# Kernel optimization log

Hardware: AMD Instinct MI355X
Metric: run time of the kernel (lower is better)

Reference implementation:

```python
import jax, jax.numpy as jnp
import numpy as np

N = 100_000      # nodes
E = 1_600_000    # edges (avg degree 16)
D_IN = 128
D_OUT = 128
K = 64           # low-rank attention rank


def setup_inputs() -> dict:
    key = jax.random.key(0)
    ks = jax.random.split(key, 6)
    s = lambda d: 1.0 / np.sqrt(d)
    return {
        "x": jax.random.normal(ks[0], (N, D_IN), dtype=jnp.float32),
        "edge_index": jax.random.randint(ks[1], (2, E), 0, N, dtype=jnp.int32),
        "W_gcn": jax.random.normal(ks[2], (D_IN, D_OUT), dtype=jnp.float32) * s(D_IN),
        "b_gcn": jnp.zeros((D_OUT,), jnp.float32),
        "W_att": jax.random.normal(ks[3], (D_IN, 4 * K), dtype=jnp.float32) * s(D_IN),
        "b_att": jnp.zeros((4 * K,), jnp.float32),
        "W_red": jax.random.normal(ks[4], (D_OUT + 2 * K, D_OUT), dtype=jnp.float32) * s(D_OUT + 2 * K),
        "b_red": jnp.zeros((D_OUT,), jnp.float32),
    }


def _forward(x, W_gcn, b_gcn, W_att, b_att, W_red, b_red, edge_index):
    n = x.shape[0]
    # --- GCN conv (symmetric normalization, self-loops), dropout = identity (eval) ---
    loop = jnp.arange(n, dtype=edge_index.dtype)
    src = jnp.concatenate([edge_index[0], loop])
    dst = jnp.concatenate([edge_index[1], loop])
    deg = jax.ops.segment_sum(jnp.ones_like(dst, dtype=x.dtype), dst, num_segments=n)
    dinv = jax.lax.rsqrt(deg)                      # deg >= 1 due to self-loops
    norm = dinv[src] * dinv[dst]                   # [E+n]
    h = x @ W_gcn                                  # [n, D_OUT]
    agg = jax.ops.segment_sum(h[src] * norm[:, None], dst, num_segments=n) + b_gcn
    x_local = jax.nn.relu(agg)

    # --- Low-rank global attention (LRGA) ---
    t = jax.nn.relu(x @ W_att + b_att)             # [n, 4K]
    U, V, Z, T = jnp.split(t, 4, axis=1)           # each [n, K]
    # joint_normalize2: scalar 1/mean(U @ (V^T @ 1_n))
    D = 1.0 / jnp.mean(U @ (V.T @ jnp.ones((n, 1), x.dtype)))
    res = (U @ (V.T @ Z)) * D                      # [n, K]
    x_global = jnp.concatenate([res, T], axis=1)   # [n, 2K]

    # --- fuse + dim reduce ---
    return jnp.concatenate([x_local, x_global], axis=1) @ W_red + b_red


def reference(x, edge_index, W_gcn, b_gcn, W_att, b_att, W_red, b_red):
    return _forward(x, W_gcn, b_gcn, W_att, b_att, W_red, b_red, edge_index)
```

## Files before the change

kernel.cpp:

```cpp
#include <hip/hip_runtime.h>

#define DIN   128
#define DOUT  128
#define KR    64
#define TCOLS 256
#define WCOLS 384
#define P_RED 1024
#define PSTR  4224
#define STCAP 6144

typedef unsigned short ushort_t;
typedef __attribute__((ext_vector_type(8))) short bf16x8;
typedef __attribute__((ext_vector_type(4))) float f32x4;

__device__ __forceinline__ float bf2f(unsigned short u) {
  return __uint_as_float(((unsigned int)u) << 16);
}
__device__ __forceinline__ unsigned short f2bf(float f) {
  unsigned int b = __float_as_uint(f);
  b = b + 0x7FFFu + ((b >> 16) & 1u);
  return (unsigned short)(b >> 16);
}

__global__ __launch_bounds__(256) void k_init(int* __restrict__ degc, float* __restrict__ VtZ,
                                              float* __restrict__ colsum, int* __restrict__ bcur,
                                              int* __restrict__ ocnt, int N) {
  int i = blockIdx.x * 256 + threadIdx.x;
  if (i < N) degc[i] = 1;
  if (i < 4096) VtZ[i] = 0.f;
  if (i < 128) colsum[i] = 0.f;
  if (i < 128) bcur[i] = 0;
  if (i == 0) ocnt[0] = 0;
}

__global__ __launch_bounds__(256) void k_deg(const int* __restrict__ ei, int* __restrict__ degc, int E) {
  int e = blockIdx.x * 256 + threadIdx.x;
  if (e < E) atomicAdd(&degc[ei[E + e]], 1);
}

__global__ __launch_bounds__(256) void k_split(const float* __restrict__ x,
                                               ushort_t* __restrict__ xhF, ushort_t* __restrict__ xloF,
                                               int N, int total_slots) {
  int gid = blockIdx.x * 256 + threadIdx.x;
  int stride = gridDim.x * 256;
  for (; gid < total_slots; gid += stride) {
    int f = gid >> 6, l = gid & 63;
    int r16 = f >> 2, s = f & 3;
    int row = r16 * 16 + (l & 15);
    int k = s * 32 + ((l >> 4) << 3);
    ushort4 h0, h1, l0, l1;
    if (row < N) {
      float4 a = *(const float4*)&x[(size_t)row * DIN + k];
      float4 b = *(const float4*)&x[(size_t)row * DIN + k + 4];
      h0.x = f2bf(a.x); h0.y = f2bf(a.y); h0.z = f2bf(a.z); h0.w = f2bf(a.w);
      h1.x = f2bf(b.x); h1.y = f2bf(b.y); h1.z = f2bf(b.z); h1.w = f2bf(b.w);
      l0.x = f2bf(a.x - bf2f(h0.x)); l0.y = f2bf(a.y - bf2f(h0.y));
      l0.z = f2bf(a.z - bf2f(h0.z)); l0.w = f2bf(a.w - bf2f(h0.w));
      l1.x = f2bf(b.x - bf2f(h1.x)); l1.y = f2bf(b.y - bf2f(h1.y));
      l1.z = f2bf(b.z - bf2f(h1.z)); l1.w = f2bf(b.w - bf2f(h1.w));
    } else {
      h0 = make_ushort4(0, 0, 0, 0); h1 = h0; l0 = h0; l1 = h0;
    }
    ((ushort4*)xhF)[gid * 2] = h0;
    ((ushort4*)xhF)[gid * 2 + 1] = h1;
    ((ushort4*)xloF)[gid * 2] = l0;
    ((ushort4*)xloF)[gid * 2 + 1] = l1;
  }
}

__global__ __launch_bounds__(256) void k_wprep(const float* __restrict__ Wg, const float* __restrict__ Wa,
                                               ushort_t* __restrict__ whF, ushort_t* __restrict__ wlF) {
  int g = blockIdx.x * 256 + threadIdx.x;
  int f = g >> 6, l = g & 63;
  int c16 = f >> 2, s = f & 3;
  int col = c16 * 16 + (l & 15);
  int k = s * 32 + ((l >> 4) << 3);
#pragma unroll
  for (int j = 0; j < 8; ++j) {
    float v = (col < DOUT) ? Wg[(size_t)(k + j) * DOUT + col]
                           : Wa[(size_t)(k + j) * TCOLS + (col - DOUT)];
    ushort_t h = f2bf(v);
    whF[(size_t)g * 8 + j] = h;
    wlF[(size_t)g * 8 + j] = f2bf(v - bf2f(h));
  }
}

__global__ __launch_bounds__(256) void k_scan1(const int* __restrict__ degc, int* __restrict__ offs,
                                               int* __restrict__ bsums, int N) {
  __shared__ int s[256];
  int tid = threadIdx.x;
  int base = blockIdx.x * 1024 + tid * 4;
  int c[4], e[4];
#pragma unroll
  for (int q = 0; q < 4; ++q) c[q] = (base + q < N) ? (degc[base + q] - 1) : 0;
  e[0] = 0; e[1] = c[0]; e[2] = e[1] + c[1]; e[3] = e[2] + c[2];
  int tsum = e[3] + c[3];
  s[tid] = tsum; __syncthreads();
  for (int off = 1; off < 256; off <<= 1) {
    int v = (tid >= off) ? s[tid - off] : 0;
    __syncthreads();
    s[tid] += v;
    __syncthreads();
  }
  int tb = s[tid] - tsum;
#pragma unroll
  for (int q = 0; q < 4; ++q) if (base + q < N) offs[base + q] = tb + e[q];
  if (tid == 255) bsums[blockIdx.x] = s[255];
}

__global__ __launch_bounds__(128) void k_scan2(const int* __restrict__ bsums, int* __restrict__ boff,
                                               int* __restrict__ offs, int NBLK, int N) {
  __shared__ int s[128];
  int tid = threadIdx.x;
  int v = (tid < NBLK) ? bsums[tid] : 0;
  s[tid] = v; __syncthreads();
  for (int off = 1; off < 128; off <<= 1) {
    int u = (tid >= off) ? s[tid - off] : 0;
    __syncthreads();
    s[tid] += u;
    __syncthreads();
  }
  boff[tid] = s[tid] - v;
  if (tid == 127) offs[N] = s[127];
}

__global__ __launch_bounds__(256) void k_scan3(int* __restrict__ offs, const int* __restrict__ boff,
                                               const int* __restrict__ degc, float* __restrict__ dinv,
                                               int* __restrict__ cursor, int N) {
  int i = blockIdx.x * 256 + threadIdx.x;
  if (i < N) {
    offs[i] += boff[i >> 10];
    dinv[i] = rsqrtf((float)degc[i]);
    cursor[i] = 0;
  }
}

__global__ __launch_bounds__(256) void k_bin(const int* __restrict__ ei, int* __restrict__ bcur,
                                             int2* __restrict__ buckets,
                                             int2* __restrict__ oflow, int* __restrict__ ocnt,
                                             int E, int B, int CAP) {
  __shared__ int hist[128], pref[128], place[128], gbase[128];
  __shared__ int2 st[4096];
  int tid = threadIdx.x;
  int e0 = blockIdx.x * 4096;
  int nE = min(4096, E - e0);
  if (nE <= 0) return;

  if (tid < 128) { hist[tid] = 0; place[tid] = 0; }
  __syncthreads();

  int src[16], dst[16];
#pragma unroll
  for (int q = 0; q < 16; ++q) {
    int idx = tid + q * 256;
    if (idx < nE) {
      src[q] = ei[e0 + idx];
      dst[q] = ei[E + e0 + idx];
      atomicAdd(&hist[dst[q] >> 10], 1);
    }
  }
  __syncthreads();

  if (tid < 128) pref[tid] = hist[tid];
  __syncthreads();
  for (int off = 1; off < 128; off <<= 1) {
    int v = (tid < 128 && tid >= off) ? pref[tid - off] : 0;
    __syncthreads();
    if (tid < 128) pref[tid] += v;
    __syncthreads();
  }
  if (tid < 128) pref[tid] -= hist[tid];
  if (tid < B && hist[tid] > 0) gbase[tid] = atomicAdd(&bcur[tid], hist[tid]);
  __syncthreads();

#pragma unroll
  for (int q = 0; q < 16; ++q) {
    int idx = tid + q * 256;
    if (idx < nE) {
      int b = dst[q] >> 10;
      int p = pref[b] + atomicAdd(&place[b], 1);
      st[p] = make_int2(src[q], dst[q]);
    }
  }
  __syncthreads();

  for (int i = tid; i < nE; i += 256) {
    int2 q = st[i];
    int b = q.y >> 10;
    int gp = gbase[b] + (i - pref[b]);
    if (gp < CAP) {
      buckets[(size_t)b * CAP + gp] = q;
    } else {
      int oi = atomicAdd(ocnt, 1);
      oflow[oi] = q;
    }
  }
}

__global__ __launch_bounds__(256) void k_scatter2(const int2* __restrict__ buckets,
                                                  const int* __restrict__ bcur,
                                                  const int* __restrict__ offs,
                                                  const float* __restrict__ dinv,
                                                  int* __restrict__ cursor,
                                                  int2* __restrict__ csr, int CAP, int N) {
  __shared__ int lcur[256];
  __shared__ int2 st[STCAP];
  int cb = blockIdx.x >> 2;
  int lo = cb * 1024 + (blockIdx.x & 3) * 256;
  if (lo >= N) return;
  int tid = threadIdx.x;
  int nnode = min(256, N - lo);
  int base = offs[lo];
  int nb = offs[lo + nnode] - base;
  if (tid < nnode) lcur[tid] = offs[lo + tid];
  __syncthreads();
  int avail = min(bcur[cb], CAP);
  const int2* sp = &buckets[(size_t)cb * CAP];
  bool staged = (nb <= STCAP);
  int quarter = lo >> 8;
  for (int i = tid; i < avail; i += 256) {
    int2 q = sp[i];
    if ((q.y >> 8) != quarter) continue;
    int p = atomicAdd(&lcur[q.y - lo], 1);
    int2 c;
    c.x = q.x;
    c.y = __float_as_int(dinv[q.x] * dinv[q.y]);
    if (staged) st[p - base] = c;
    else        csr[p] = c;
  }
  __syncthreads();
  if (staged) {
    for (int i = tid; i < nb; i += 256) csr[base + i] = st[i];
  }
  if (tid < nnode) cursor[lo + tid] = lcur[tid];
}

__global__ __launch_bounds__(256) void k_fixup(const int2* __restrict__ oflow, const int* __restrict__ ocnt,
                                               int* __restrict__ cursor, const float* __restrict__ dinv,
                                               int2* __restrict__ csr) {
  int n = ocnt[0];
  for (int i = blockIdx.x * 256 + threadIdx.x; i < n; i += gridDim.x * 256) {
    int2 q = oflow[i];
    int pos = atomicAdd(&cursor[q.y], 1);
    int2 c;
    c.x = q.x;
    c.y = __float_as_int(dinv[q.x] * dinv[q.y]);
    csr[pos] = c;
  }
}

#define LOADK(S, AH, AL, BH, BL)                                              \
  {                                                                           \
    _Pragma("unroll") for (int m_ = 0; m_ < 4; ++m_) {                        \
      size_t fo_ = (((size_t)(r16b + m_) * 4 + (S)) * 64 + lane) * 8;         \
      AH[m_] = *(const bf16x8*)&xhF[fo_];                                     \
      AL[m_] = *(const bf16x8*)&xloF[fo_];                                    \
    }                                                                         \
    _Pragma("unroll") for (int n_ = 0; n_ < 4; ++n_) {                        \
      size_t fo_ = (((size_t)(c16b + n_) * 4 + (S)) * 64 + lane) * 8;         \
      BH[n_] = *(const bf16x8*)&whF[fo_];                                     \
      BL[n_] = *(const bf16x8*)&wlF[fo_];                                     \
    }                                                                         \
  }

__global__ __launch_bounds__(256) void k_gemm1_mfma(const ushort_t* __restrict__ xhF,
                                                    const ushort_t* __restrict__ xloF,
                                                    const ushort_t* __restrict__ whF,
                                                    const ushort_t* __restrict__ wlF,
                                                    const float* __restrict__ ba,
                                                    ushort_t* __restrict__ hs, ushort_t* __restrict__ t,
                                                    int N, int ntiles) {
  int bid = blockIdx.x;
  int g = bid / 24;
  int rem = bid - g * 24;
  int colblk = rem >> 3;
  int ytile = g * 8 + (rem & 7);
  if (ytile >= ntiles) return;

  int tid = threadIdx.x;
  int lane = tid & 63;
  int wave = tid >> 6;
  int wr = wave >> 1, wc = wave & 1;
  int rowbase = ytile * 128 + wr * 64;
  int gcb = colblk * 128 + wc * 64;
  int r16b = ytile * 8 + wr * 4;
  int c16b = colblk * 8 + wc * 4;
  int lr = lane & 15;
  int rq = (lane >> 4) * 4;

  f32x4 acc[4][4] = {};
  bf16x8 ah[2][4], al[2][4], bh[2][4], bl[2][4];

  LOADK(0, ah[0], al[0], bh[0], bl[0]);
#pragma unroll
  for (int s = 0; s < 4; ++s) {
    int cur = s & 1, nxt = cur ^ 1;
    if (s < 3) LOADK(s + 1, ah[nxt], al[nxt], bh[nxt], bl[nxt]);
#pragma unroll
    for (int m = 0; m < 4; ++m)
#pragma unroll
      for (int n = 0; n < 4; ++n) {
        acc[m][n] = __builtin_amdgcn_mfma_f32_16x16x32_bf16(ah[cur][m], bl[cur][n], acc[m][n], 0, 0, 0);
        acc[m][n] = __builtin_amdgcn_mfma_f32_16x16x32_bf16(al[cur][m], bh[cur][n], acc[m][n], 0, 0, 0);
        acc[m][n] = __builtin_amdgcn_mfma_f32_16x16x32_bf16(ah[cur][m], bh[cur][n], acc[m][n], 0, 0, 0);
      }
  }

  if (colblk == 0) {
#pragma unroll
    for (int m = 0; m < 4; ++m)
#pragma unroll
      for (int i = 0; i < 4; ++i) {
        int row = rowbase + m * 16 + rq + i;
        if (row < N) {
#pragma unroll
          for (int n = 0; n < 4; ++n)
            hs[(size_t)row * DOUT + gcb + n * 16 + lr] = f2bf(acc[m][n][i]);
        }
      }
  } else {
    float bav[4];
#pragma unroll
    for (int n = 0; n < 4; ++n) bav[n] = ba[gcb - DOUT + n * 16 + lr];
#pragma unroll
    for (int m = 0; m < 4; ++m)
#pragma unroll
      for (int i = 0; i < 4; ++i) {
        int row = rowbase + m * 16 + rq + i;
        if (row < N) {
#pragma unroll
          for (int n = 0; n < 4; ++n)
            t[(size_t)row * TCOLS + gcb - DOUT + n * 16 + lr] =
                f2bf(fmaxf(acc[m][n][i] + bav[n], 0.f));
        }
      }
  }
}

__global__ __launch_bounds__(256) void k_red(const ushort_t* __restrict__ t, float* __restrict__ part,
                                             int N) {
  __shared__ ushort_t ts[32 * 200];
  __shared__ float csh[512];
  int tid = threadIdx.x;
  int lane = tid & 63;
  int w = tid >> 6;
  int lr = lane & 15;
  int lk = (lane >> 4) * 8;
  int vcol = 64 + w * 16 + lr;
  int col2 = lane * 2;

  f32x4 acc[4] = {};
  float cs0 = 0.f, cs1 = 0.f;
  int ntiles = (N + 31) >> 5;

  for (int tile = blockIdx.x; tile < ntiles; tile += gridDim.x) {
    int r0 = tile * 32;
    for (int i = tid; i < 768; i += 256) {
      int r = i / 24, c0 = (i % 24) * 8;
      int row = r0 + r;
      ushort4 v0, v1;
      if (row < N) {
        v0 = ((const ushort4*)&t[(size_t)row * TCOLS + c0])[0];
        v1 = ((const ushort4*)&t[(size_t)row * TCOLS + c0])[1];
      } else {
        v0 = make_ushort4(0, 0, 0, 0); v1 = v0;
      }
      *(ushort4*)&ts[r * 200 + c0] = v0;
      *(ushort4*)&ts[r * 200 + c0 + 4] = v1;
    }
    __syncthreads();
    bf16x8 a, b[4];
#pragma unroll
    for (int j = 0; j < 8; ++j)
      ((ushort_t*)&a)[j] = ts[(lk + j) * 200 + vcol];
#pragma unroll
    for (int n = 0; n < 4; ++n)
#pragma unroll
      for (int j = 0; j < 8; ++j)
        ((ushort_t*)&b[n])[j] = ts[(lk + j) * 200 + 128 + n * 16 + lr];
#pragma unroll
    for (int j = 0; j < 8; ++j) {
      ushort2 u = *(const ushort2*)&ts[(w * 8 + j) * 200 + col2];
      cs0 += bf2f(u.x); cs1 += bf2f(u.y);
    }
#pragma unroll
    for (int n = 0; n < 4; ++n)
      acc[n] = __builtin_amdgcn_mfma_f32_16x16x32_bf16(a, b[n], acc[n], 0, 0, 0);
    __syncthreads();
  }

  float* pb = &part[(size_t)blockIdx.x * PSTR];
  int rq = (lane >> 4) * 4;
#pragma unroll
  for (int n = 0; n < 4; ++n)
#pragma unroll
    for (int i = 0; i < 4; ++i)
      pb[(w * 16 + rq + i) * 64 + n * 16 + lr] = acc[n][i];

  csh[tid] = cs0;
  csh[256 + tid] = cs1;
  __syncthreads();
  if (w == 0) {
    float t0 = csh[lane] + csh[64 + lane] + csh[128 + lane] + csh[192 + lane];
    float t1 = csh[256 + lane] + csh[320 + lane] + csh[384 + lane] + csh[448 + lane];
    pb[4096 + col2] = t0;
    pb[4096 + col2 + 1] = t1;
  }
}

__global__ __launch_bounds__(256) void k_redsum(const float* __restrict__ part,
                                                float* __restrict__ VtZ, float* __restrict__ colsum) {
  __shared__ float s[256];
  int tid = threadIdx.x;
  int j = blockIdx.x * 64 + (tid & 63);
  int bc = tid >> 6;
  float a = 0.f;
#pragma unroll 4
  for (int b = bc; b < P_RED; b += 4) a += part[(size_t)b * PSTR + j];
  s[tid] = a;
  __syncthreads();
  if (bc == 0) {
    float v = s[tid] + s[tid + 64] + s[tid + 128] + s[tid + 192];
    if (j < 4096) VtZ[j] = v;
    else colsum[j - 4096] = v;
  }
}

__global__ __launch_bounds__(64) void k_d(const float* __restrict__ colsum, float* __restrict__ Dws, int N) {
  __shared__ float s[64];
  int k = threadIdx.x;
  s[k] = colsum[k] * colsum[64 + k];
  __syncthreads();
  for (int off = 32; off > 0; off >>= 1) {
    if (k < off) s[k] += s[k + off];
    __syncthreads();
  }
  if (k == 0) {
    float p = s[0];
    Dws[0] = (p != 0.f) ? ((float)N / p) : 0.f;
  }
}

__global__ __launch_bounds__(256) void k_prep(const float* __restrict__ VtZ,
                                              const float* __restrict__ Dws,
                                              const float* __restrict__ Wr,
                                              ushort_t* __restrict__ weffF) {
  int g = blockIdx.x * 256 + threadIdx.x;
  int f = g >> 6, l = g & 63;
  int c16 = f >> 3, s = f & 7;
  int c = c16 * 16 + (l & 15);
  int k0 = s * 32 + ((l >> 4) << 3);
  float Dv = Dws[0];
#pragma unroll
  for (int j = 0; j < 8; ++j) {
    int k = k0 + j;
    float v;
    if (k < 128 || k >= 192) {
      v = Wr[(size_t)k * DOUT + c];
    } else {
      int kk = k - 128;
      float acc = 0.f;
      for (int q = 0; q < 64; ++q)
        acc += VtZ[kk * 64 + q] * Wr[(size_t)(128 + q) * DOUT + c];
      v = acc * Dv;
    }
    weffF[(size_t)g * 8 + j] = f2bf(v);
  }
}

__global__ __launch_bounds__(256) void k_out_mfma(const ushort_t* __restrict__ xl,
                                                  const ushort_t* __restrict__ t,
                                                  const ushort_t* __restrict__ weffF,
                                                  const float* __restrict__ br,
                                                  float* __restrict__ out, int N) {
  __shared__ ushort_t ys[32 * 264];
  int tid = threadIdx.x;
  int lane = tid & 63;
  int w = tid >> 6;
  int lr = lane & 15;
  int lk = (lane >> 4) * 8;
  int rq = (lane >> 4) * 4;
  int r0 = blockIdx.x * 32;

  for (int i = tid; i < 1024; i += 256) {
    int r = i >> 5, c0 = (i & 31) * 8;
    int row = r0 + r;
    ushort4 v0, v1;
    if (row < N) {
      const ushort_t* src;
      if (c0 < 128)      src = &xl[(size_t)row * DOUT + c0];
      else if (c0 < 192) src = &t[(size_t)row * TCOLS + (c0 - 128)];
      else               src = &t[(size_t)row * TCOLS + c0];
      v0 = ((const ushort4*)src)[0];
      v1 = ((const ushort4*)src)[1];
    } else {
      v0 = make_ushort4(0, 0, 0, 0); v1 = v0;
    }
    *(ushort4*)&ys[r * 264 + c0] = v0;
    *(ushort4*)&ys[r * 264 + c0 + 4] = v1;
  }
  __syncthreads();

  f32x4 acc[2][2] = {};
#pragma unroll
  for (int s = 0; s < 8; ++s) {
    bf16x8 a[2], b[2];
#pragma unroll
    for (int m = 0; m < 2; ++m)
      a[m] = *(const bf16x8*)&ys[(m * 16 + lr) * 264 + s * 32 + lk];
#pragma unroll
    for (int n = 0; n < 2; ++n) {
      int f = (w * 2 + n) * 8 + s;
      b[n] = *(const bf16x8*)&weffF[((size_t)f * 64 + lane) * 8];
    }
#pragma unroll
    for (int m = 0; m < 2; ++m)
#pragma unroll
      for (int n = 0; n < 2; ++n)
        acc[m][n] = __builtin_amdgcn_mfma_f32_16x16x32_bf16(a[m], b[n], acc[m][n], 0, 0, 0);
  }

  float brv[2];
#pragma unroll
  for (int n = 0; n < 2; ++n) brv[n] = br[w * 32 + n * 16 + lr];
#pragma unroll
  for (int m = 0; m < 2; ++m)
#pragma unroll
    for (int i = 0; i < 4; ++i) {
      int row = r0 + m * 16 + rq + i;
      if (row < N) {
#pragma unroll
        for (int n = 0; n < 2; ++n)
          out[(size_t)row * DOUT + w * 32 + n * 16 + lr] = acc[m][n][i] + brv[n];
      }
    }
}

__global__ __launch_bounds__(256) void k_aggn(const ushort_t* __restrict__ hs, const int2* __restrict__ csr,
                                              const int* __restrict__ offs, const float* __restrict__ dinv,
                                              const float* __restrict__ bg,
                                              ushort_t* __restrict__ xl, int N) {
  int node = blockIdx.x * 4 + (threadIdx.x >> 6);
  int lane = threadIdx.x & 63;
  if (node >= N) return;
  int c2 = 2 * lane;
  float dn = dinv[node];
  ushort2 u = *(const ushort2*)&hs[(size_t)node * DOUT + c2];
  float a0 = dn * dn * bf2f(u.x);
  float a1 = dn * dn * bf2f(u.y);
  int e = offs[node], e1 = offs[node + 1];
  for (; e + 4 <= e1; e += 4) {
    int2 q0 = csr[e], q1 = csr[e + 1], q2 = csr[e + 2], q3 = csr[e + 3];
    ushort2 r0 = *(const ushort2*)&hs[(size_t)q0.x * DOUT + c2];
    ushort2 r1 = *(const ushort2*)&hs[(size_t)q1.x * DOUT + c2];
    ushort2 r2 = *(const ushort2*)&hs[(size_t)q2.x * DOUT + c2];
    ushort2 r3 = *(const ushort2*)&hs[(size_t)q3.x * DOUT + c2];
    float n0 = __int_as_float(q0.y), n1 = __int_as_float(q1.y);
    float n2 = __int_as_float(q2.y), n3 = __int_as_float(q3.y);
    a0 += n0 * bf2f(r0.x) + n1 * bf2f(r1.x) + n2 * bf2f(r2.x) + n3 * bf2f(r3.x);
    a1 += n0 * bf2f(r0.y) + n1 * bf2f(r1.y) + n2 * bf2f(r2.y) + n3 * bf2f(r3.y);
  }
  for (; e < e1; ++e) {
    int2 q = csr[e];
    ushort2 r = *(const ushort2*)&hs[(size_t)q.x * DOUT + c2];
    float n0 = __int_as_float(q.y);
    a0 += n0 * bf2f(r.x);
    a1 += n0 * bf2f(r.y);
  }
  ushort2 o;
  o.x = f2bf(fmaxf(a0 + bg[c2], 0.f));
  o.y = f2bf(fmaxf(a1 + bg[c2 + 1], 0.f));
  *(ushort2*)&xl[(size_t)node * DOUT + c2] = o;
}

extern "C" void kernel_launch(void* const* d_in, const int* in_sizes, int n_in,
                              void* d_out, int out_size, void* d_ws, size_t ws_size,
                              hipStream_t stream) {
  const float* x  = (const float*)d_in[0];
  const int* ei   = (const int*)d_in[1];
  const float* Wg = (const float*)d_in[2];
  const float* bg = (const float*)d_in[3];
  const float* Wa = (const float*)d_in[4];
  const float* ba = (const float*)d_in[5];
  const float* Wr = (const float*)d_in[6];
  const float* br = (const float*)d_in[7];
  float* out = (float*)d_out;

  const int N = in_sizes[0] / DIN;
  const int E = in_sizes[1] / 2;

  const int NT128 = (N + 127) / 128;
  const int N16P = NT128 * 8;
  const int NFRAG_A = N16P * 4;
  const int B = (N + 1023) >> 10;
  const int CAP = ((E / (B > 0 ? B : 1)) * 3 / 2 + 255) & ~255;

  char* p = (char*)d_ws;
  auto alloc = [&](size_t bytes) {
    char* r = p;
    p += (bytes + 255) & ~(size_t)255;
    return r;
  };
  float* Dws    = (float*)alloc(256);
  float* colsum = (float*)alloc(128 * 4);
  float* VtZ    = (float*)alloc(4096 * 4);
  int*   bsums  = (int*)alloc(1024);
  int*   boff   = (int*)alloc(1024);
  int*   bcur   = (int*)alloc(1024);
  int*   ocnt   = (int*)alloc(256);
  ushort_t* weffF = (ushort_t*)alloc(128 * 256 * 2);
  ushort_t* whF = (ushort_t*)alloc((size_t)24 * 4 * 512 * 2);
  ushort_t* wlF = (ushort_t*)alloc((size_t)24 * 4 * 512 * 2);
  float* part   = (float*)alloc((size_t)P_RED * PSTR * 4);
  int*   degc   = (int*)alloc((size_t)N * 4);
  float* dinv   = (float*)alloc((size_t)N * 4);
  int*   offs   = (int*)alloc((size_t)(N + 1) * 4);
  int*   cursor = (int*)alloc((size_t)N * 4);
  int2*  csr    = (int2*)alloc((size_t)E * 8);
  int2*  buckets= (int2*)alloc((size_t)B * CAP * 8);
  int2*  oflow  = (int2*)alloc((size_t)E * 8);
  ushort_t* xhF = (ushort_t*)alloc((size_t)NFRAG_A * 512 * 2);
  ushort_t* xloF= (ushort_t*)alloc((size_t)NFRAG_A * 512 * 2);
  ushort_t* hs  = (ushort_t*)alloc((size_t)N * DOUT * 2);
  ushort_t* t   = (ushort_t*)alloc((size_t)N * TCOLS * 2);
  ushort_t* xl  = (ushort_t*)alloc((size_t)N * DOUT * 2);
  (void)ws_size; (void)n_in; (void)out_size;

  const int GN = (N + 255) / 256;
  const int GE = (E + 255) / 256;
  const int NBLK = (N + 1023) / 1024;
  const int G1 = ((NT128 + 7) / 8) * 24;
  const int GBIN = (E + 4095) / 4096;
  const int NT32 = (N + 31) / 32;

  k_init<<<GN, 256, 0, stream>>>(degc, VtZ, colsum, bcur, ocnt, N);
  k_deg<<<GE, 256, 0, stream>>>(ei, degc, E);
  k_split<<<2048, 256, 0, stream>>>(x, xhF, xloF, N, NFRAG_A * 64);
  k_wprep<<<24, 256, 0, stream>>>(Wg, Wa, whF, wlF);
  k_scan1<<<NBLK, 256, 0, stream>>>(degc, offs, bsums, N);
  k_scan2<<<1, 128, 0, stream>>>(bsums, boff, offs, NBLK, N);
  k_scan3<<<GN, 256, 0, stream>>>(offs, boff, degc, dinv, cursor, N);
  k_bin<<<GBIN, 256, 0, stream>>>(ei, bcur, buckets, oflow, ocnt, E, B, CAP);
  k_scatter2<<<B * 4, 256, 0, stream>>>(buckets, bcur, offs, dinv, cursor, csr, CAP, N);
  k_fixup<<<32, 256, 0, stream>>>(oflow, ocnt, cursor, dinv, csr);
  k_gemm1_mfma<<<G1, 256, 0, stream>>>(xhF, xloF, whF, wlF, ba, hs, t, N, NT128);
  k_red<<<P_RED, 256, 0, stream>>>(t, part, N);
  k_redsum<<<PSTR / 64, 256, 0, stream>>>(part, VtZ, colsum);
  k_d<<<1, 64, 0, stream>>>(colsum, Dws, N);
  k_prep<<<16, 256, 0, stream>>>(VtZ, Dws, Wr, weffF);
  k_aggn<<<(N + 3) / 4, 256, 0, stream>>>(hs, csr, offs, dinv, bg, xl, N);
  k_out_mfma<<<NT32, 256, 0, stream>>>(xl, t, weffF, br, out, N);
}
```

Before: 446.0 us.

## Fuse degree count into binning and aggregation into output GEMM

The degree atomics move into k_bin, which now runs before the scan, so the separate k_deg pass over the edge list goes away. The GCN neighbor aggregation is fused into the output MFMA kernel: each block aggregates its 32 rows directly into shared memory instead of writing and re-reading the bf16 x_local buffer. This removes two launches and one intermediate round trip through global memory. In exchange the gather now runs at 32 rows per block with 8 serial rows per wave, which lowers parallelism for the latency-bound gather.

```diff
diff --git a/kernel.cpp b/kernel.cpp
--- a/kernel.cpp
+++ b/kernel.cpp
@@ -31,11 +31,6 @@
   if (i < 128) colsum[i] = 0.f;
   if (i < 128) bcur[i] = 0;
   if (i == 0) ocnt[0] = 0;
-}
-
-__global__ __launch_bounds__(256) void k_deg(const int* __restrict__ ei, int* __restrict__ degc, int E) {
-  int e = blockIdx.x * 256 + threadIdx.x;
-  if (e < E) atomicAdd(&degc[ei[E + e]], 1);
 }
 
 __global__ __launch_bounds__(256) void k_split(const float* __restrict__ x,
@@ -136,6 +131,7 @@
 }
 
 __global__ __launch_bounds__(256) void k_bin(const int* __restrict__ ei, int* __restrict__ bcur,
+                                             int* __restrict__ degc,
                                              int2* __restrict__ buckets,
                                              int2* __restrict__ oflow, int* __restrict__ ocnt,
                                              int E, int B, int CAP) {
@@ -157,6 +153,7 @@
       src[q] = ei[e0 + idx];
       dst[q] = ei[E + e0 + idx];
       atomicAdd(&hist[dst[q] >> 10], 1);
+      atomicAdd(&degc[dst[q]], 1);
     }
   }
   __syncthreads();
@@ -468,11 +465,15 @@
   }
 }
 
-__global__ __launch_bounds__(256) void k_out_mfma(const ushort_t* __restrict__ xl,
-                                                  const ushort_t* __restrict__ t,
-                                                  const ushort_t* __restrict__ weffF,
-                                                  const float* __restrict__ br,
-                                                  float* __restrict__ out, int N) {
+__global__ __launch_bounds__(256) void k_aggout(const ushort_t* __restrict__ hs,
+                                                const int2* __restrict__ csr,
+                                                const int* __restrict__ offs,
+                                                const float* __restrict__ dinv,
+                                                const float* __restrict__ bg,
+                                                const ushort_t* __restrict__ t,
+                                                const ushort_t* __restrict__ weffF,
+                                                const float* __restrict__ br,
+                                                float* __restrict__ out, int N) {
   __shared__ ushort_t ys[32 * 264];
   int tid = threadIdx.x;
   int lane = tid & 63;
@@ -481,16 +482,50 @@
   int lk = (lane >> 4) * 8;
   int rq = (lane >> 4) * 4;
   int r0 = blockIdx.x * 32;
-
-  for (int i = tid; i < 1024; i += 256) {
-    int r = i >> 5, c0 = (i & 31) * 8;
+  int c2 = 2 * lane;
+
+  float bg0 = bg[c2], bg1 = bg[c2 + 1];
+  for (int q = 0; q < 8; ++q) {
+    int r = w * 8 + q;
+    int node = r0 + r;
+    ushort2 o = make_ushort2(0, 0);
+    if (node < N) {
+      float dn = dinv[node];
+      ushort2 u = *(const ushort2*)&hs[(size_t)node * DOUT + c2];
+      float a0 = dn * dn * bf2f(u.x);
+      float a1 = dn * dn * bf2f(u.y);
+      int e = offs[node], e1 = offs[node + 1];
+      for (; e + 4 <= e1; e += 4) {
+        int2 q0 = csr[e], q1 = csr[e + 1], q2 = csr[e + 2], q3 = csr[e + 3];
+        ushort2 r0v = *(const ushort2*)&hs[(size_t)q0.x * DOUT + c2];
+        ushort2 r1v = *(const ushort2*)&hs[(size_t)q1.x * DOUT + c2];
+        ushort2 r2v = *(const ushort2*)&hs[(size_t)q2.x * DOUT + c2];
+        ushort2 r3v = *(const ushort2*)&hs[(size_t)q3.x * DOUT + c2];
+        float n0 = __int_as_float(q0.y), n1 = __int_as_float(q1.y);
+        float n2 = __int_as_float(q2.y), n3 = __int_as_float(q3.y);
+        a0 += n0 * bf2f(r0v.x) + n1 * bf2f(r1v.x) + n2 * bf2f(r2v.x) + n3 * bf2f(r3v.x);
+        a1 += n0 * bf2f(r0v.y) + n1 * bf2f(r1v.y) + n2 * bf2f(r2v.y) + n3 * bf2f(r3v.y);
+      }
+      for (; e < e1; ++e) {
+        int2 qe = csr[e];
+        ushort2 rv = *(const ushort2*)&hs[(size_t)qe.x * DOUT + c2];
+        float n0 = __int_as_float(qe.y);
+        a0 += n0 * bf2f(rv.x);
+        a1 += n0 * bf2f(rv.y);
+      }
+      o.x = f2bf(fmaxf(a0 + bg0, 0.f));
+      o.y = f2bf(fmaxf(a1 + bg1, 0.f));
+    }
+    *(ushort2*)&ys[r * 264 + c2] = o;
+  }
+
+  for (int i = tid; i < 512; i += 256) {
+    int r = i >> 4, c0 = 128 + (i & 15) * 8;
     int row = r0 + r;
     ushort4 v0, v1;
     if (row < N) {
-      const ushort_t* src;
-      if (c0 < 128)      src = &xl[(size_t)row * DOUT + c0];
-      else if (c0 < 192) src = &t[(size_t)row * TCOLS + (c0 - 128)];
-      else               src = &t[(size_t)row * TCOLS + c0];
+      const ushort_t* src = (c0 < 192) ? &t[(size_t)row * TCOLS + (c0 - 128)]
+                                       : &t[(size_t)row * TCOLS + c0];
       v0 = ((const ushort4*)src)[0];
       v1 = ((const ushort4*)src)[1];
     } else {
@@ -534,43 +569,6 @@
           out[(size_t)row * DOUT + w * 32 + n * 16 + lr] = acc[m][n][i] + brv[n];
       }
     }
-}
-
-__global__ __launch_bounds__(256) void k_aggn(const ushort_t* __restrict__ hs, const int2* __restrict__ csr,
-                                              const int* __restrict__ offs, const float* __restrict__ dinv,
-                                              const float* __restrict__ bg,
-                                              ushort_t* __restrict__ xl, int N) {
-  int node = blockIdx.x * 4 + (threadIdx.x >> 6);
-  int lane = threadIdx.x & 63;
-  if (node >= N) return;
-  int c2 = 2 * lane;
-  float dn = dinv[node];
-  ushort2 u = *(const ushort2*)&hs[(size_t)node * DOUT + c2];
-  float a0 = dn * dn * bf2f(u.x);
-  float a1 = dn * dn * bf2f(u.y);
-  int e = offs[node], e1 = offs[node + 1];
-  for (; e + 4 <= e1; e += 4) {
-    int2 q0 = csr[e], q1 = csr[e + 1], q2 = csr[e + 2], q3 = csr[e + 3];
-    ushort2 r0 = *(const ushort2*)&hs[(size_t)q0.x * DOUT + c2];
-    ushort2 r1 = *(const ushort2*)&hs[(size_t)q1.x * DOUT + c2];
-    ushort2 r2 = *(const ushort2*)&hs[(size_t)q2.x * DOUT + c2];
-    ushort2 r3 = *(const ushort2*)&hs[(size_t)q3.x * DOUT + c2];
-    float n0 = __int_as_float(q0.y), n1 = __int_as_float(q1.y);
-    float n2 = __int_as_float(q2.y), n3 = __int_as_float(q3.y);
-    a0 += n0 * bf2f(r0.x) + n1 * bf2f(r1.x) + n2 * bf2f(r2.x) + n3 * bf2f(r3.x);
-    a1 += n0 * bf2f(r0.y) + n1 * bf2f(r1.y) + n2 * bf2f(r2.y) + n3 * bf2f(r3.y);
-  }
-  for (; e < e1; ++e) {
-    int2 q = csr[e];
-    ushort2 r = *(const ushort2*)&hs[(size_t)q.x * DOUT + c2];
-    float n0 = __int_as_float(q.y);
-    a0 += n0 * bf2f(r.x);
-    a1 += n0 * bf2f(r.y);
-  }
-  ushort2 o;
-  o.x = f2bf(fmaxf(a0 + bg[c2], 0.f));
-  o.y = f2bf(fmaxf(a1 + bg[c2 + 1], 0.f));
-  *(ushort2*)&xl[(size_t)node * DOUT + c2] = o;
 }
 
 extern "C" void kernel_launch(void* const* d_in, const int* in_sizes, int n_in,
@@ -623,24 +621,21 @@
   ushort_t* xloF= (ushort_t*)alloc((size_t)NFRAG_A * 512 * 2);
   ushort_t* hs  = (ushort_t*)alloc((size_t)N * DOUT * 2);
   ushort_t* t   = (ushort_t*)alloc((size_t)N * TCOLS * 2);
-  ushort_t* xl  = (ushort_t*)alloc((size_t)N * DOUT * 2);
   (void)ws_size; (void)n_in; (void)out_size;
 
   const int GN = (N + 255) / 256;
-  const int GE = (E + 255) / 256;
   const int NBLK = (N + 1023) / 1024;
   const int G1 = ((NT128 + 7) / 8) * 24;
   const int GBIN = (E + 4095) / 4096;
   const int NT32 = (N + 31) / 32;
 
   k_init<<<GN, 256, 0, stream>>>(degc, VtZ, colsum, bcur, ocnt, N);
-  k_deg<<<GE, 256, 0, stream>>>(ei, degc, E);
+  k_bin<<<GBIN, 256, 0, stream>>>(ei, bcur, degc, buckets, oflow, ocnt, E, B, CAP);
   k_split<<<2048, 256, 0, stream>>>(x, xhF, xloF, N, NFRAG_A * 64);
   k_wprep<<<24, 256, 0, stream>>>(Wg, Wa, whF, wlF);
   k_scan1<<<NBLK, 256, 0, stream>>>(degc, offs, bsums, N);
   k_scan2<<<1, 128, 0, stream>>>(bsums, boff, offs, NBLK, N);
   k_scan3<<<GN, 256, 0, stream>>>(offs, boff, degc, dinv, cursor, N);
-  k_bin<<<GBIN, 256, 0, stream>>>(ei, bcur, buckets, oflow, ocnt, E, B, CAP);
   k_scatter2<<<B * 4, 256, 0, stream>>>(buckets, bcur, offs, dinv, cursor, csr, CAP, N);
   k_fixup<<<32, 256, 0, stream>>>(oflow, ocnt, cursor, dinv, csr);
   k_gemm1_mfma<<<G1, 256, 0, stream>>>(xhF, xloF, whF, wlF, ba, hs, t, N, NT128);
@@ -648,6 +643,5 @@
   k_redsum<<<PSTR / 64, 256, 0, stream>>>(part, VtZ, colsum);
   k_d<<<1, 64, 0, stream>>>(colsum, Dws, N);
   k_prep<<<16, 256, 0, stream>>>(VtZ, Dws, Wr, weffF);
-  k_aggn<<<(N + 3) / 4, 256, 0, stream>>>(hs, csr, offs, dinv, bg, xl, N);
-  k_out_mfma<<<NT32, 256, 0, stream>>>(xl, t, weffF, br, out, N);
-}
+  k_aggout<<<NT32, 256, 0, stream>>>(hs, csr, offs, dinv, bg, t, weffF, br, out, N);
+}
```

New measurement: 428.0 us. -4.0%, faster.
